# Kernel tuning notes

Hardware: AMD Instinct MI355X
Metric: run time of the kernel (lower is better)

The kernel has to match this reference:

```python
import jax, jax.numpy as jnp
import numpy as np

N_HEAD = 16
ROPE_BASE = 10000.0


def _rope_tables(T, head_dim, dtype):
    # RotaryEmbedding(dim=head_dim//2): inv_freq over arange(0, dim, 2)/dim
    rot = head_dim // 2  # 32
    inv_freq = 1.0 / (ROPE_BASE ** (jnp.arange(0, rot, 2, dtype=jnp.float32) / rot))  # [rot/2]
    pos = jnp.arange(T, dtype=jnp.float32)
    freqs = jnp.outer(pos, inv_freq)                     # [T, rot/2]
    emb = jnp.concatenate([freqs, freqs], axis=-1)       # [T, rot]
    return jnp.cos(emb).astype(dtype), jnp.sin(emb).astype(dtype)


def _apply_rope(q, k, cos, sin):
    # q,k: [B,H,T,hd]; cos,sin: [T, hd//2] broadcast over B,H
    hd = q.shape[-1]
    half = hd // 2
    cos = cos[None, None]
    sin = sin[None, None]
    q1, q2 = q[..., :half], q[..., half:]
    k1, k2 = k[..., :half], k[..., half:]
    q_rot = jnp.concatenate([q1 * cos - q2 * sin, q2 * cos + q1 * sin], axis=-1)
    k_rot = jnp.concatenate([k1 * cos - k2 * sin, k2 * cos + k1 * sin], axis=-1)
    return q_rot, k_rot


def setup_inputs() -> dict:
    key = jax.random.key(0)
    ks = jax.random.split(key, 4)
    B, T, C = 4, 2048, 1024
    x = jax.random.normal(ks[0], (B, T, C), dtype=jnp.float32)
    W_attn = jax.random.normal(ks[1], (C, 3 * C), dtype=jnp.float32) * (1.0 / np.sqrt(C))
    b_attn = jnp.zeros((3 * C,), dtype=jnp.float32)
    W_proj = jax.random.normal(ks[2], (C, C), dtype=jnp.float32) * (1.0 / np.sqrt(C))
    b_proj = jnp.zeros((C,), dtype=jnp.float32)
    return {"x": x, "W_attn": W_attn, "b_attn": b_attn, "W_proj": W_proj, "b_proj": b_proj}


def reference(x, W_attn, b_attn, W_proj, b_proj):
    B, T, C = x.shape
    H = N_HEAD
    hd = C // H
    qkv = x @ W_attn + b_attn                            # [B,T,3C]
    q, k, v = jnp.split(qkv, 3, axis=-1)
    # [B,T,C] -> [B,H,T,hd]
    q = q.reshape(B, T, H, hd).transpose(0, 2, 1, 3)
    k = k.reshape(B, T, H, hd).transpose(0, 2, 1, 3)
    v = v.reshape(B, T, H, hd).transpose(0, 2, 1, 3)
    cos, sin = _rope_tables(T, hd, x.dtype)
    q, k = _apply_rope(q, k, cos, sin)
    att = jnp.einsum("bhqd,bhkd->bhqk", q, k) * (1.0 / np.sqrt(hd))
    causal = jnp.tril(jnp.ones((T, T), dtype=bool))
    att = jnp.where(causal[None, None], att, jnp.float32(-jnp.inf).astype(att.dtype))
    att = jax.nn.softmax(att, axis=-1)
    y = jnp.einsum("bhqk,bhkd->bhqd", att, v)            # [B,H,T,hd]
    y = y.transpose(0, 2, 1, 3).reshape(B, T, C)
    return y @ W_proj + b_proj
```

## Files before the change

kernel.cpp:

```cpp
#include <hip/hip_runtime.h>
#include <math.h>


typedef unsigned short u16;
typedef __bf16 bf16x8 __attribute__((ext_vector_type(8)));
typedef float f32x4 __attribute__((ext_vector_type(4)));
typedef float f32x16 __attribute__((ext_vector_type(16)));

__device__ __forceinline__ float b2f(u16 x) {
  union { unsigned u; float f; } c; c.u = ((unsigned)x) << 16; return c.f;
}
__device__ __forceinline__ u16 f2b(float f) {
  union { __bf16 h; u16 u; } c; c.h = (__bf16)f; return c.u;
}

__global__ __launch_bounds__(256) void sentinel_k(u16* __restrict__ out, int n) {
  int i = blockIdx.x * 256 + threadIdx.x;
  if (i < n) out[i] = 0x4480;
}

__global__ __launch_bounds__(256) void transpose_f2b_k(const float* __restrict__ src,
                                                       u16* __restrict__ dst,
                                                       int R, int C) {
  __shared__ u16 tile[64][65];
  int tc = blockIdx.x * 64, tr = blockIdx.y * 64;
  int t = threadIdx.x;
  int rr = t >> 3;
  int c8 = (t & 7) * 8;
#pragma unroll
  for (int i = 0; i < 2; ++i) {
    int r = rr + i * 32;
    f32x4 p0 = *(const f32x4*)(src + (long)(tr + r) * C + tc + c8);
    f32x4 p1 = *(const f32x4*)(src + (long)(tr + r) * C + tc + c8 + 4);
#pragma unroll
    for (int j = 0; j < 4; ++j) {
      tile[r][c8 + j] = f2b(p0[j]);
      tile[r][c8 + 4 + j] = f2b(p1[j]);
    }
  }
  __syncthreads();
#pragma unroll
  for (int i = 0; i < 2; ++i) {
    int a = rr + i * 32;
    u16 vv[8];
#pragma unroll
    for (int j = 0; j < 8; ++j) vv[j] = tile[c8 + j][a];
    *(uint4*)(dst + (long)(tc + a) * R + tr + c8) = *(uint4*)vv;
  }
}

__global__ __launch_bounds__(256) void transpose_b_k(const u16* __restrict__ src,
                                                     u16* __restrict__ dst,
                                                     int R, int C,
                                                     long sBatch, long dBatch) {
  __shared__ u16 tile[64][65];
  src += (long)blockIdx.z * sBatch;
  dst += (long)blockIdx.z * dBatch;
  int tc = blockIdx.x * 64, tr = blockIdx.y * 64;
  int t = threadIdx.x;
  int rr = t >> 3;
  int c8 = (t & 7) * 8;
#pragma unroll
  for (int i = 0; i < 2; ++i) {
    int r = rr + i * 32;
    uint4 v = *(const uint4*)(src + (long)(tr + r) * C + tc + c8);
    u16 vv[8]; *(uint4*)vv = v;
#pragma unroll
    for (int j = 0; j < 8; ++j) tile[r][c8 + j] = vv[j];
  }
  __syncthreads();
#pragma unroll
  for (int i = 0; i < 2; ++i) {
    int a = rr + i * 32;
    u16 vv[8];
#pragma unroll
    for (int j = 0; j < 8; ++j) vv[j] = tile[c8 + j][a];
    *(uint4*)(dst + (long)(tc + a) * R + tr + c8) = *(uint4*)vv;
  }
}

__global__ void rope_table_k(float2* __restrict__ tab) {
  int i = blockIdx.x * 256 + threadIdx.x;
  if (i >= 2048 * 16) return;
  int t = i >> 4, f = i & 15;
  float invf = exp2f(-(float)f * (13.287712379549449f / 16.0f));
  float th = (float)t * invf;
  float s, c;
  sincosf(th, &s, &c);
  tab[i] = make_float2(c, s);
}

__global__ __launch_bounds__(256) void rope_apply_k(u16* __restrict__ Qg,
                                                    u16* __restrict__ Kg,
                                                    const float2* __restrict__ tab) {
  const float QSCALE = 0.18033688501389543f;
  long tid = (long)blockIdx.x * 256 + threadIdx.x;
  int j = (int)(tid & 7);
  long row = tid >> 3;
  int t = (int)(row & 2047);
  int d0 = j * 4;
  u16* qp = Qg + row * 64;
  u16* kp = Kg + row * 64;
  u16 a1[4], a2[4], b1[4], b2[4];
  *(ushort4*)a1 = *(ushort4*)(qp + d0);
  *(ushort4*)a2 = *(ushort4*)(qp + d0 + 32);
  *(ushort4*)b1 = *(ushort4*)(kp + d0);
  *(ushort4*)b2 = *(ushort4*)(kp + d0 + 32);
  const float2* tp = tab + t * 16 + (d0 & 15);
#pragma unroll
  for (int i = 0; i < 4; ++i) {
    float2 cs = tp[i];
    float x1 = b2f(a1[i]), x2 = b2f(a2[i]);
    float y1 = b2f(b1[i]), y2 = b2f(b2[i]);
    a1[i] = f2b((x1 * cs.x - x2 * cs.y) * QSCALE);
    a2[i] = f2b((x2 * cs.x + x1 * cs.y) * QSCALE);
    b1[i] = f2b(y1 * cs.x - y2 * cs.y);
    b2[i] = f2b(y2 * cs.x + y1 * cs.y);
  }
  *(ushort4*)(qp + d0) = *(ushort4*)a1;
  *(ushort4*)(qp + d0 + 32) = *(ushort4*)a2;
  *(ushort4*)(kp + d0) = *(ushort4*)b1;
  *(ushort4*)(kp + d0 + 32) = *(ushort4*)b2;
}

template <int MODE>
__global__ __launch_bounds__(256) void gemm_k(const void* __restrict__ Av,
                                              const u16* __restrict__ Bt,
                                              const float* __restrict__ bias,
                                              void* __restrict__ outv,
                                              int M, int N, int K) {
  __shared__ u16 As[128 * 40];
  __shared__ u16 Bs[128 * 40];
  int tid = threadIdx.x, wid = tid >> 6, lane = tid & 63;
  int wr = wid >> 1, wc = wid & 1;
  long m0 = (long)blockIdx.x * 128, n0 = (long)blockIdx.y * 128;
  int r = lane & 15, g = lane >> 4;
  long arow = m0 + wid * 32 + (lane >> 2);
  int acol = (lane & 3) * 8;
  const float* Agf = (const float*)Av + arow * (long)K + acol;
  const u16*   Agb = (const u16*)Av + arow * (long)K + acol;
  const u16* Bg = Bt + (n0 + wid * 32 + (lane >> 2)) * (long)K + acol;
  int lrow = wid * 32 + (lane >> 2);
  int lcol = acol;
  f32x4 acc[4][4] = {};
  int nk = K >> 5;
  for (int kt = 0; kt < nk; ++kt) {
    long ko = (long)kt * 32;
    uint4 a0, a1;
    if (MODE == 1) {
      f32x4 p0 = *(const f32x4*)(Agf + ko);
      f32x4 p1 = *(const f32x4*)(Agf + ko + 4);
      f32x4 p2 = *(const f32x4*)(Agf + ko + 16 * (long)K);
      f32x4 p3 = *(const f32x4*)(Agf + ko + 16 * (long)K + 4);
      u16 h0[8], h1[8];
#pragma unroll
      for (int j = 0; j < 4; ++j) {
        h0[j] = f2b(p0[j]); h0[4 + j] = f2b(p1[j]);
        h1[j] = f2b(p2[j]); h1[4 + j] = f2b(p3[j]);
      }
      a0 = *(uint4*)h0; a1 = *(uint4*)h1;
    } else {
      a0 = *(const uint4*)(Agb + ko);
      a1 = *(const uint4*)(Agb + ko + 16 * (long)K);
    }
    uint4 b0 = *(const uint4*)(Bg + ko);
    uint4 b1 = *(const uint4*)(Bg + ko + 16 * (long)K);
    __syncthreads();
    *(uint4*)&As[lrow * 40 + lcol] = a0;
    *(uint4*)&As[(lrow + 16) * 40 + lcol] = a1;
    *(uint4*)&Bs[lrow * 40 + lcol] = b0;
    *(uint4*)&Bs[(lrow + 16) * 40 + lcol] = b1;
    __syncthreads();
    bf16x8 af[4], bfr[4];
#pragma unroll
    for (int mt = 0; mt < 4; ++mt)
      af[mt] = *(const bf16x8*)&As[(wr * 64 + mt * 16 + r) * 40 + g * 8];
#pragma unroll
    for (int nt = 0; nt < 4; ++nt)
      bfr[nt] = *(const bf16x8*)&Bs[(wc * 64 + nt * 16 + r) * 40 + g * 8];
#pragma unroll
    for (int mt = 0; mt < 4; ++mt)
#pragma unroll
      for (int nt = 0; nt < 4; ++nt)
        acc[mt][nt] = __builtin_amdgcn_mfma_f32_16x16x32_bf16(af[mt], bfr[nt], acc[mt][nt], 0, 0, 0);
  }
#pragma unroll
  for (int nt = 0; nt < 4; ++nt) {
    long col = n0 + wc * 64 + nt * 16 + r;
    float bv = bias[col];
#pragma unroll
    for (int mt = 0; mt < 4; ++mt) {
#pragma unroll
      for (int e = 0; e < 4; ++e) {
        long row = m0 + wr * 64 + mt * 16 + g * 4 + e;
        float v = acc[mt][nt][e] + bv;
        if (MODE == 0) {
          ((float*)outv)[row * N + col] = v;
        } else {
          int which = (int)(col >> 10);
          int cc = (int)col & 1023;
          int hh = cc >> 6, dd = cc & 63;
          long bb = row >> 11;
          int tt = (int)row & 2047;
          ((u16*)outv)[(long)which * 8388608 + (((bb * 16 + hh) * 2048 + tt) << 6) + dd] = f2b(v);
        }
      }
    }
  }
}

__global__ __launch_bounds__(256) void attn_k(const u16* __restrict__ Qg,
                                              const u16* __restrict__ Kg,
                                              const u16* __restrict__ VgT,
                                              u16* __restrict__ Y) {
  __shared__ u16 Ks[64 * 72];
  __shared__ u16 Vt[64 * 72];
  int qb = 15 - (int)blockIdx.y;
  int bh = blockIdx.x;
  int b = bh >> 4, h = bh & 15;
  long base = (long)bh * (2048 * 64);
  int tid = threadIdx.x, wid = tid >> 6;
  int lane = tid & 63, l31 = lane & 31, hi = lane >> 5;
  int q0w = qb * 128 + wid * 32;
  int myEnd = (q0w + 31) >> 6;
  int ktMax = 2 * qb + 1;
  bf16x8 qf[4];
  {
    const u16* qp = Qg + base + (long)(q0w + l31) * 64 + hi * 8;
#pragma unroll
    for (int s = 0; s < 4; ++s) qf[s] = *(const bf16x8*)(qp + s * 16);
  }
  f32x16 acc0 = {}, acc1 = {};
  float mrow = -INFINITY, lrow = 0.f;
  for (int kt = 0; kt <= ktMax; ++kt) {
    __syncthreads();
#pragma unroll
    for (int uu = 0; uu < 2; ++uu) {
      int u = tid + uu * 256;
      int row = u >> 3, c4 = (u & 7) * 8;
      *(uint4*)&Ks[row * 72 + c4] =
          *(const uint4*)&Kg[base + (long)(kt * 64 + row) * 64 + c4];
      *(uint4*)&Vt[row * 72 + c4] =
          *(const uint4*)&VgT[base + (long)row * 2048 + kt * 64 + c4];
    }
    __syncthreads();
    if (kt > myEnd) continue;
    f32x16 st[2];
#pragma unroll
    for (int ct = 0; ct < 2; ++ct) {
      f32x16 z = {};
#pragma unroll
      for (int s = 0; s < 4; ++s) {
        bf16x8 kf = *(const bf16x8*)&Ks[(ct * 32 + l31) * 72 + s * 16 + hi * 8];
        z = __builtin_amdgcn_mfma_f32_32x32x16_bf16(kf, qf[s], z, 0, 0, 0);
      }
      st[ct] = z;
    }
    if (kt == myEnd) {
      int qg = q0w + l31;
#pragma unroll
      for (int ct = 0; ct < 2; ++ct)
#pragma unroll
        for (int reg = 0; reg < 16; ++reg) {
          int kg = kt * 64 + ct * 32 + (reg & 3) + 8 * (reg >> 2) + 4 * hi;
          if (kg > qg) st[ct][reg] = -INFINITY;
        }
    }
    float t8[8];
#pragma unroll
    for (int i = 0; i < 8; ++i)
      t8[i] = fmaxf(fmaxf(st[0][i], st[0][i + 8]), fmaxf(st[1][i], st[1][i + 8]));
#pragma unroll
    for (int i = 0; i < 4; ++i) t8[i] = fmaxf(t8[i], t8[i + 4]);
    float pm = fmaxf(fmaxf(t8[0], t8[1]), fmaxf(t8[2], t8[3]));
    pm = fmaxf(pm, __shfl_xor(pm, 32));
    if (__any(pm > mrow + 8.0f)) {
      float mn = fmaxf(mrow, pm);
      float alpha = exp2f(mrow - mn);
      mrow = mn;
      lrow *= alpha;
#pragma unroll
      for (int reg = 0; reg < 16; ++reg) {
        float aB = __shfl(alpha, (reg & 3) + 8 * (reg >> 2) + 4 * hi);
        acc0[reg] *= aB;
        acc1[reg] *= aB;
      }
    }
    float s8[8];
#pragma unroll
    for (int i = 0; i < 8; ++i) s8[i] = 0.f;
#pragma unroll
    for (int ct = 0; ct < 2; ++ct)
#pragma unroll
      for (int reg = 0; reg < 16; ++reg) {
        float p = exp2f(st[ct][reg] - mrow);
        st[ct][reg] = p;
        s8[reg & 7] += p;
      }
#pragma unroll
    for (int i = 0; i < 4; ++i) s8[i] += s8[i + 4];
    float rs = (s8[0] + s8[1]) + (s8[2] + s8[3]);
    rs += __shfl_xor(rs, 32);
    lrow += rs;
#pragma unroll
    for (int ct = 0; ct < 2; ++ct) {
      bf16x8 af[2];
#pragma unroll
      for (int ks = 0; ks < 2; ++ks) {
#pragma unroll
        for (int u = 0; u < 4; ++u) {
          float sendv = hi ? st[ct][8 * ks + u] : st[ct][8 * ks + 4 + u];
          float keepv = hi ? st[ct][8 * ks + 4 + u] : st[ct][8 * ks + u];
          float rcv = __shfl_xor(sendv, 32);
          af[ks][u] = (__bf16)(hi ? rcv : keepv);
          af[ks][4 + u] = (__bf16)(hi ? keepv : rcv);
        }
      }
#pragma unroll
      for (int ks = 0; ks < 2; ++ks) {
        bf16x8 vf0 = *(const bf16x8*)&Vt[l31 * 72 + ct * 32 + ks * 16 + hi * 8];
        bf16x8 vf1 = *(const bf16x8*)&Vt[(32 + l31) * 72 + ct * 32 + ks * 16 + hi * 8];
        acc0 = __builtin_amdgcn_mfma_f32_32x32x16_bf16(af[ks], vf0, acc0, 0, 0, 0);
        acc1 = __builtin_amdgcn_mfma_f32_32x32x16_bf16(af[ks], vf1, acc1, 0, 0, 0);
      }
    }
  }
  float rinv = 1.0f / lrow;
#pragma unroll
  for (int reg = 0; reg < 16; ++reg) {
    int crow = (reg & 3) + 8 * (reg >> 2) + 4 * hi;
    float rB = __shfl(rinv, crow);
    long orow = (long)(b * 2048 + q0w + crow) * 1024 + h * 64;
    Y[orow + l31] = f2b(acc0[reg] * rB);
    Y[orow + 32 + l31] = f2b(acc1[reg] * rB);
  }
}

extern "C" void kernel_launch(void* const* d_in, const int* in_sizes, int n_in,
                              void* d_out, int out_size, void* d_ws, size_t ws_size,
                              hipStream_t stream) {
  const float* x  = (const float*)d_in[0];
  const float* Wa = (const float*)d_in[1];
  const float* ba = (const float*)d_in[2];
  const float* Wp = (const float*)d_in[3];
  const float* bp = (const float*)d_in[4];

  if (ws_size < 67108864ULL) {
    sentinel_k<<<dim3((out_size + 255) / 256), 256, 0, stream>>>((u16*)d_out, out_size);
    return;
  }

  u16* ws  = (u16*)d_ws;
  u16* Qg  = ws;
  u16* Kg  = ws + 8388608;
  u16* Vg  = ws + 16777216;
  u16* Yb  = ws + 16777216;
  u16* WaT = ws + 25165824;
  float2* tab = (float2*)(ws + 28311552);
  u16* VgT = ws + 25165824;
  u16* WpT = ws;

  transpose_f2b_k<<<dim3(48, 16), 256, 0, stream>>>(Wa, WaT, 1024, 3072);
  rope_table_k<<<dim3(128), 256, 0, stream>>>(tab);
  gemm_k<1><<<dim3(64, 24), 256, 0, stream>>>(x, WaT, ba, Qg, 8192, 3072, 1024);
  rope_apply_k<<<dim3(4096), 256, 0, stream>>>(Qg, Kg, tab);
  transpose_b_k<<<dim3(1, 32, 64), 256, 0, stream>>>(Vg, VgT, 2048, 64, 131072L, 131072L);
  attn_k<<<dim3(64, 16), 256, 0, stream>>>(Qg, Kg, VgT, Yb);
  transpose_f2b_k<<<dim3(16, 16), 256, 0, stream>>>(Wp, WpT, 1024, 1024);
  gemm_k<0><<<dim3(64, 8), 256, 0, stream>>>(Yb, WpT, bp, d_out, 8192, 1024, 1024);
}
```

Before: 224.9 us.

## Fuse RoPE into QKV GEMM, pair causal q-strips, use direct-to-LDS loads

Folds the RoPE rotation and Q scaling into the QKV GEMM epilogue, which removes the separate rope_apply pass that read and rewrote Q and K. The attention kernel now gives each wave two 32-row query strips, one near the start and one near the end of the sequence, to balance causal work across blocks, and halves the grid. The output projection GEMM switches to global_load_lds for direct global-to-LDS copies with an unpadded layout. The risks are LDS bank conflicts from dropping the padding, higher register pressure in attention, and an extra barrier per k-step in the projection GEMM.

```diff
diff --git a/kernel.cpp b/kernel.cpp
--- a/kernel.cpp
+++ b/kernel.cpp
@@ -7,12 +7,19 @@
 typedef float f32x4 __attribute__((ext_vector_type(4)));
 typedef float f32x16 __attribute__((ext_vector_type(16)));
 
+#define QSCALE 0.18033688501389543f
+
 __device__ __forceinline__ float b2f(u16 x) {
   union { unsigned u; float f; } c; c.u = ((unsigned)x) << 16; return c.f;
 }
 __device__ __forceinline__ u16 f2b(float f) {
   union { __bf16 h; u16 u; } c; c.h = (__bf16)f; return c.u;
 }
+
+#define GLOAD16(gp, lp)                                                  \
+  __builtin_amdgcn_global_load_lds(                                      \
+      (const __attribute__((address_space(1))) unsigned int*)(gp),       \
+      (__attribute__((address_space(3))) unsigned int*)(lp), 16, 0, 0)
 
 __global__ __launch_bounds__(256) void sentinel_k(u16* __restrict__ out, int n) {
   int i = blockIdx.x * 256 + threadIdx.x;
@@ -90,45 +97,12 @@
   tab[i] = make_float2(c, s);
 }
 
-__global__ __launch_bounds__(256) void rope_apply_k(u16* __restrict__ Qg,
-                                                    u16* __restrict__ Kg,
-                                                    const float2* __restrict__ tab) {
-  const float QSCALE = 0.18033688501389543f;
-  long tid = (long)blockIdx.x * 256 + threadIdx.x;
-  int j = (int)(tid & 7);
-  long row = tid >> 3;
-  int t = (int)(row & 2047);
-  int d0 = j * 4;
-  u16* qp = Qg + row * 64;
-  u16* kp = Kg + row * 64;
-  u16 a1[4], a2[4], b1[4], b2[4];
-  *(ushort4*)a1 = *(ushort4*)(qp + d0);
-  *(ushort4*)a2 = *(ushort4*)(qp + d0 + 32);
-  *(ushort4*)b1 = *(ushort4*)(kp + d0);
-  *(ushort4*)b2 = *(ushort4*)(kp + d0 + 32);
-  const float2* tp = tab + t * 16 + (d0 & 15);
-#pragma unroll
-  for (int i = 0; i < 4; ++i) {
-    float2 cs = tp[i];
-    float x1 = b2f(a1[i]), x2 = b2f(a2[i]);
-    float y1 = b2f(b1[i]), y2 = b2f(b2[i]);
-    a1[i] = f2b((x1 * cs.x - x2 * cs.y) * QSCALE);
-    a2[i] = f2b((x2 * cs.x + x1 * cs.y) * QSCALE);
-    b1[i] = f2b(y1 * cs.x - y2 * cs.y);
-    b2[i] = f2b(y2 * cs.x + y1 * cs.y);
-  }
-  *(ushort4*)(qp + d0) = *(ushort4*)a1;
-  *(ushort4*)(qp + d0 + 32) = *(ushort4*)a2;
-  *(ushort4*)(kp + d0) = *(ushort4*)b1;
-  *(ushort4*)(kp + d0 + 32) = *(ushort4*)b2;
-}
-
-template <int MODE>
-__global__ __launch_bounds__(256) void gemm_k(const void* __restrict__ Av,
-                                              const u16* __restrict__ Bt,
-                                              const float* __restrict__ bias,
-                                              void* __restrict__ outv,
-                                              int M, int N, int K) {
+__global__ __launch_bounds__(256) void gemm_qkv_k(const float* __restrict__ A,
+                                                  const u16* __restrict__ Bt,
+                                                  const float* __restrict__ bias,
+                                                  const float2* __restrict__ tab,
+                                                  u16* __restrict__ out,
+                                                  int M, int N, int K) {
   __shared__ u16 As[128 * 40];
   __shared__ u16 Bs[128 * 40];
   int tid = threadIdx.x, wid = tid >> 6, lane = tid & 63;
@@ -137,8 +111,7 @@
   int r = lane & 15, g = lane >> 4;
   long arow = m0 + wid * 32 + (lane >> 2);
   int acol = (lane & 3) * 8;
-  const float* Agf = (const float*)Av + arow * (long)K + acol;
-  const u16*   Agb = (const u16*)Av + arow * (long)K + acol;
+  const float* Agf = A + arow * (long)K + acol;
   const u16* Bg = Bt + (n0 + wid * 32 + (lane >> 2)) * (long)K + acol;
   int lrow = wid * 32 + (lane >> 2);
   int lcol = acol;
@@ -146,23 +119,17 @@
   int nk = K >> 5;
   for (int kt = 0; kt < nk; ++kt) {
     long ko = (long)kt * 32;
-    uint4 a0, a1;
-    if (MODE == 1) {
-      f32x4 p0 = *(const f32x4*)(Agf + ko);
-      f32x4 p1 = *(const f32x4*)(Agf + ko + 4);
-      f32x4 p2 = *(const f32x4*)(Agf + ko + 16 * (long)K);
-      f32x4 p3 = *(const f32x4*)(Agf + ko + 16 * (long)K + 4);
-      u16 h0[8], h1[8];
-#pragma unroll
-      for (int j = 0; j < 4; ++j) {
-        h0[j] = f2b(p0[j]); h0[4 + j] = f2b(p1[j]);
-        h1[j] = f2b(p2[j]); h1[4 + j] = f2b(p3[j]);
-      }
-      a0 = *(uint4*)h0; a1 = *(uint4*)h1;
-    } else {
-      a0 = *(const uint4*)(Agb + ko);
-      a1 = *(const uint4*)(Agb + ko + 16 * (long)K);
-    }
+    f32x4 p0 = *(const f32x4*)(Agf + ko);
+    f32x4 p1 = *(const f32x4*)(Agf + ko + 4);
+    f32x4 p2 = *(const f32x4*)(Agf + ko + 16 * (long)K);
+    f32x4 p3 = *(const f32x4*)(Agf + ko + 16 * (long)K + 4);
+    u16 h0[8], h1[8];
+#pragma unroll
+    for (int j = 0; j < 4; ++j) {
+      h0[j] = f2b(p0[j]); h0[4 + j] = f2b(p1[j]);
+      h1[j] = f2b(p2[j]); h1[4 + j] = f2b(p3[j]);
+    }
+    uint4 a0 = *(uint4*)h0, a1 = *(uint4*)h1;
     uint4 b0 = *(const uint4*)(Bg + ko);
     uint4 b1 = *(const uint4*)(Bg + ko + 16 * (long)K);
     __syncthreads();
@@ -184,55 +151,119 @@
       for (int nt = 0; nt < 4; ++nt)
         acc[mt][nt] = __builtin_amdgcn_mfma_f32_16x16x32_bf16(af[mt], bfr[nt], acc[mt][nt], 0, 0, 0);
   }
+  int which = (int)(n0 >> 10);
+  int hh = ((int)(n0 & 1023) >> 6) + wc;
+  float bv[4];
+#pragma unroll
+  for (int nt = 0; nt < 4; ++nt) bv[nt] = bias[n0 + wc * 64 + nt * 16 + r];
+#pragma unroll
+  for (int mt = 0; mt < 4; ++mt) {
+#pragma unroll
+    for (int e = 0; e < 4; ++e) {
+      long row = m0 + wr * 64 + mt * 16 + g * 4 + e;
+      long bb = row >> 11;
+      int tt = (int)row & 2047;
+      float v0 = acc[mt][0][e] + bv[0];
+      float v1 = acc[mt][1][e] + bv[1];
+      float v2 = acc[mt][2][e] + bv[2];
+      float v3 = acc[mt][3][e] + bv[3];
+      if (which < 2) {
+        float2 cs = tab[tt * 16 + r];
+        float r0 = v0 * cs.x - v2 * cs.y, r2 = v2 * cs.x + v0 * cs.y;
+        float r1 = v1 * cs.x - v3 * cs.y, r3 = v3 * cs.x + v1 * cs.y;
+        if (which == 0) { r0 *= QSCALE; r1 *= QSCALE; r2 *= QSCALE; r3 *= QSCALE; }
+        v0 = r0; v1 = r1; v2 = r2; v3 = r3;
+      }
+      u16* op = out + (long)which * 8388608 + (((bb * 16 + hh) * 2048 + tt) << 6);
+      op[r] = f2b(v0);
+      op[16 + r] = f2b(v1);
+      op[32 + r] = f2b(v2);
+      op[48 + r] = f2b(v3);
+    }
+  }
+}
+
+__global__ __launch_bounds__(256) void gemm_proj_k(const u16* __restrict__ A,
+                                                   const u16* __restrict__ Bt,
+                                                   const float* __restrict__ bias,
+                                                   float* __restrict__ out,
+                                                   int M, int N, int K) {
+  __shared__ u16 As[128 * 32];
+  __shared__ u16 Bs[128 * 32];
+  int tid = threadIdx.x, wid = tid >> 6, lane = tid & 63;
+  int wr = wid >> 1, wc = wid & 1;
+  long m0 = (long)blockIdx.x * 128, n0 = (long)blockIdx.y * 128;
+  int r = lane & 15, g = lane >> 4;
+  const u16* Ag = A + (m0 + wid * 32 + (lane >> 2)) * (long)K + (lane & 3) * 8;
+  const u16* Bg = Bt + (n0 + wid * 32 + (lane >> 2)) * (long)K + (lane & 3) * 8;
+  u16* AsW = As + wid * 1024;
+  u16* BsW = Bs + wid * 1024;
+  f32x4 acc[4][4] = {};
+  int nk = K >> 5;
+  for (int kt = 0; kt < nk; ++kt) {
+    long ko = (long)kt * 32;
+    GLOAD16(Ag + ko, AsW);
+    GLOAD16(Ag + ko + 16 * (long)K, AsW + 512);
+    GLOAD16(Bg + ko, BsW);
+    GLOAD16(Bg + ko + 16 * (long)K, BsW + 512);
+    __syncthreads();
+    bf16x8 af[4], bfr[4];
+#pragma unroll
+    for (int mt = 0; mt < 4; ++mt)
+      af[mt] = *(const bf16x8*)&As[(wr * 64 + mt * 16 + r) * 32 + g * 8];
+#pragma unroll
+    for (int nt = 0; nt < 4; ++nt)
+      bfr[nt] = *(const bf16x8*)&Bs[(wc * 64 + nt * 16 + r) * 32 + g * 8];
+#pragma unroll
+    for (int mt = 0; mt < 4; ++mt)
+#pragma unroll
+      for (int nt = 0; nt < 4; ++nt)
+        acc[mt][nt] = __builtin_amdgcn_mfma_f32_16x16x32_bf16(af[mt], bfr[nt], acc[mt][nt], 0, 0, 0);
+    __syncthreads();
+  }
 #pragma unroll
   for (int nt = 0; nt < 4; ++nt) {
     long col = n0 + wc * 64 + nt * 16 + r;
-    float bv = bias[col];
-#pragma unroll
-    for (int mt = 0; mt < 4; ++mt) {
+    float bvv = bias[col];
+#pragma unroll
+    for (int mt = 0; mt < 4; ++mt)
 #pragma unroll
       for (int e = 0; e < 4; ++e) {
         long row = m0 + wr * 64 + mt * 16 + g * 4 + e;
-        float v = acc[mt][nt][e] + bv;
-        if (MODE == 0) {
-          ((float*)outv)[row * N + col] = v;
-        } else {
-          int which = (int)(col >> 10);
-          int cc = (int)col & 1023;
-          int hh = cc >> 6, dd = cc & 63;
-          long bb = row >> 11;
-          int tt = (int)row & 2047;
-          ((u16*)outv)[(long)which * 8388608 + (((bb * 16 + hh) * 2048 + tt) << 6) + dd] = f2b(v);
-        }
-      }
-    }
-  }
-}
-
-__global__ __launch_bounds__(256) void attn_k(const u16* __restrict__ Qg,
-                                              const u16* __restrict__ Kg,
-                                              const u16* __restrict__ VgT,
-                                              u16* __restrict__ Y) {
+        out[row * N + col] = acc[mt][nt][e] + bvv;
+      }
+  }
+}
+
+__global__ __launch_bounds__(256, 2) void attn_k(const u16* __restrict__ Qg,
+                                                 const u16* __restrict__ Kg,
+                                                 const u16* __restrict__ VgT,
+                                                 u16* __restrict__ Y) {
   __shared__ u16 Ks[64 * 72];
   __shared__ u16 Vt[64 * 72];
-  int qb = 15 - (int)blockIdx.y;
+  int ib = blockIdx.y;
   int bh = blockIdx.x;
   int b = bh >> 4, h = bh & 15;
   long base = (long)bh * (2048 * 64);
   int tid = threadIdx.x, wid = tid >> 6;
   int lane = tid & 63, l31 = lane & 31, hi = lane >> 5;
-  int q0w = qb * 128 + wid * 32;
-  int myEnd = (q0w + 31) >> 6;
-  int ktMax = 2 * qb + 1;
-  bf16x8 qf[4];
+  int sA = ib * 4 + wid, sB = 63 - sA;
+  int q0A = sA * 32, q0B = sB * 32;
+  int endA = sA >> 1, endB = sB >> 1;
+  int ktEnd = 31 - 2 * ib;
+  bf16x8 qfA[4], qfB[4];
   {
-    const u16* qp = Qg + base + (long)(q0w + l31) * 64 + hi * 8;
-#pragma unroll
-    for (int s = 0; s < 4; ++s) qf[s] = *(const bf16x8*)(qp + s * 16);
-  }
-  f32x16 acc0 = {}, acc1 = {};
-  float mrow = -INFINITY, lrow = 0.f;
-  for (int kt = 0; kt <= ktMax; ++kt) {
+    const u16* qa = Qg + base + (long)(q0A + l31) * 64 + hi * 8;
+    const u16* qb = Qg + base + (long)(q0B + l31) * 64 + hi * 8;
+#pragma unroll
+    for (int s = 0; s < 4; ++s) {
+      qfA[s] = *(const bf16x8*)(qa + s * 16);
+      qfB[s] = *(const bf16x8*)(qb + s * 16);
+    }
+  }
+  f32x16 accA0 = {}, accA1 = {}, accB0 = {}, accB1 = {};
+  float mA = -INFINITY, lA = 0.f, mB = -INFINITY, lB = 0.f;
+  for (int kt = 0; kt <= ktEnd; ++kt) {
     __syncthreads();
 #pragma unroll
     for (int uu = 0; uu < 2; ++uu) {
@@ -244,96 +275,104 @@
           *(const uint4*)&VgT[base + (long)row * 2048 + kt * 64 + c4];
     }
     __syncthreads();
-    if (kt > myEnd) continue;
-    f32x16 st[2];
-#pragma unroll
-    for (int ct = 0; ct < 2; ++ct) {
-      f32x16 z = {};
-#pragma unroll
-      for (int s = 0; s < 4; ++s) {
-        bf16x8 kf = *(const bf16x8*)&Ks[(ct * 32 + l31) * 72 + s * 16 + hi * 8];
-        z = __builtin_amdgcn_mfma_f32_32x32x16_bf16(kf, qf[s], z, 0, 0, 0);
-      }
-      st[ct] = z;
-    }
-    if (kt == myEnd) {
-      int qg = q0w + l31;
+    auto tileC = [&](const bf16x8 (&qf)[4], f32x16& acc0, f32x16& acc1,
+                     float& mrow, float& lrow, int q0, int endS) {
+      f32x16 st[2];
+#pragma unroll
+      for (int ct = 0; ct < 2; ++ct) {
+        f32x16 z = {};
+#pragma unroll
+        for (int s = 0; s < 4; ++s) {
+          bf16x8 kf = *(const bf16x8*)&Ks[(ct * 32 + l31) * 72 + s * 16 + hi * 8];
+          z = __builtin_amdgcn_mfma_f32_32x32x16_bf16(kf, qf[s], z, 0, 0, 0);
+        }
+        st[ct] = z;
+      }
+      if (kt == endS) {
+        int qg = q0 + l31;
+#pragma unroll
+        for (int ct = 0; ct < 2; ++ct)
+#pragma unroll
+          for (int reg = 0; reg < 16; ++reg) {
+            int kg = kt * 64 + ct * 32 + (reg & 3) + 8 * (reg >> 2) + 4 * hi;
+            if (kg > qg) st[ct][reg] = -INFINITY;
+          }
+      }
+      float t8[8];
+#pragma unroll
+      for (int i = 0; i < 8; ++i)
+        t8[i] = fmaxf(fmaxf(st[0][i], st[0][i + 8]), fmaxf(st[1][i], st[1][i + 8]));
+#pragma unroll
+      for (int i = 0; i < 4; ++i) t8[i] = fmaxf(t8[i], t8[i + 4]);
+      float pm = fmaxf(fmaxf(t8[0], t8[1]), fmaxf(t8[2], t8[3]));
+      pm = fmaxf(pm, __shfl_xor(pm, 32));
+      if (__any(pm > mrow + 8.0f)) {
+        float mn = fmaxf(mrow, pm);
+        float alpha = exp2f(mrow - mn);
+        mrow = mn;
+        lrow *= alpha;
+#pragma unroll
+        for (int reg = 0; reg < 16; ++reg) {
+          float aB = __shfl(alpha, (reg & 3) + 8 * (reg >> 2) + 4 * hi);
+          acc0[reg] *= aB;
+          acc1[reg] *= aB;
+        }
+      }
+      float s8[8];
+#pragma unroll
+      for (int i = 0; i < 8; ++i) s8[i] = 0.f;
 #pragma unroll
       for (int ct = 0; ct < 2; ++ct)
 #pragma unroll
         for (int reg = 0; reg < 16; ++reg) {
-          int kg = kt * 64 + ct * 32 + (reg & 3) + 8 * (reg >> 2) + 4 * hi;
-          if (kg > qg) st[ct][reg] = -INFINITY;
+          float p = exp2f(st[ct][reg] - mrow);
+          st[ct][reg] = p;
+          s8[reg & 7] += p;
         }
-    }
-    float t8[8];
-#pragma unroll
-    for (int i = 0; i < 8; ++i)
-      t8[i] = fmaxf(fmaxf(st[0][i], st[0][i + 8]), fmaxf(st[1][i], st[1][i + 8]));
-#pragma unroll
-    for (int i = 0; i < 4; ++i) t8[i] = fmaxf(t8[i], t8[i + 4]);
-    float pm = fmaxf(fmaxf(t8[0], t8[1]), fmaxf(t8[2], t8[3]));
-    pm = fmaxf(pm, __shfl_xor(pm, 32));
-    if (__any(pm > mrow + 8.0f)) {
-      float mn = fmaxf(mrow, pm);
-      float alpha = exp2f(mrow - mn);
-      mrow = mn;
-      lrow *= alpha;
-#pragma unroll
-      for (int reg = 0; reg < 16; ++reg) {
-        float aB = __shfl(alpha, (reg & 3) + 8 * (reg >> 2) + 4 * hi);
-        acc0[reg] *= aB;
-        acc1[reg] *= aB;
-      }
-    }
-    float s8[8];
-#pragma unroll
-    for (int i = 0; i < 8; ++i) s8[i] = 0.f;
-#pragma unroll
-    for (int ct = 0; ct < 2; ++ct)
-#pragma unroll
-      for (int reg = 0; reg < 16; ++reg) {
-        float p = exp2f(st[ct][reg] - mrow);
-        st[ct][reg] = p;
-        s8[reg & 7] += p;
-      }
-#pragma unroll
-    for (int i = 0; i < 4; ++i) s8[i] += s8[i + 4];
-    float rs = (s8[0] + s8[1]) + (s8[2] + s8[3]);
-    rs += __shfl_xor(rs, 32);
-    lrow += rs;
-#pragma unroll
-    for (int ct = 0; ct < 2; ++ct) {
-      bf16x8 af[2];
-#pragma unroll
-      for (int ks = 0; ks < 2; ++ks) {
-#pragma unroll
-        for (int u = 0; u < 4; ++u) {
-          float sendv = hi ? st[ct][8 * ks + u] : st[ct][8 * ks + 4 + u];
-          float keepv = hi ? st[ct][8 * ks + 4 + u] : st[ct][8 * ks + u];
-          float rcv = __shfl_xor(sendv, 32);
-          af[ks][u] = (__bf16)(hi ? rcv : keepv);
-          af[ks][4 + u] = (__bf16)(hi ? keepv : rcv);
+#pragma unroll
+      for (int i = 0; i < 4; ++i) s8[i] += s8[i + 4];
+      float rs = (s8[0] + s8[1]) + (s8[2] + s8[3]);
+      rs += __shfl_xor(rs, 32);
+      lrow += rs;
+#pragma unroll
+      for (int ct = 0; ct < 2; ++ct) {
+        bf16x8 af[2];
+#pragma unroll
+        for (int ks = 0; ks < 2; ++ks) {
+#pragma unroll
+          for (int u = 0; u < 4; ++u) {
+            float sendv = hi ? st[ct][8 * ks + u] : st[ct][8 * ks + 4 + u];
+            float keepv = hi ? st[ct][8 * ks + 4 + u] : st[ct][8 * ks + u];
+            float rcv = __shfl_xor(sendv, 32);
+            af[ks][u] = (__bf16)(hi ? rcv : keepv);
+            af[ks][4 + u] = (__bf16)(hi ? keepv : rcv);
+          }
         }
-      }
-#pragma unroll
-      for (int ks = 0; ks < 2; ++ks) {
-        bf16x8 vf0 = *(const bf16x8*)&Vt[l31 * 72 + ct * 32 + ks * 16 + hi * 8];
-        bf16x8 vf1 = *(const bf16x8*)&Vt[(32 + l31) * 72 + ct * 32 + ks * 16 + hi * 8];
-        acc0 = __builtin_amdgcn_mfma_f32_32x32x16_bf16(af[ks], vf0, acc0, 0, 0, 0);
-        acc1 = __builtin_amdgcn_mfma_f32_32x32x16_bf16(af[ks], vf1, acc1, 0, 0, 0);
-      }
-    }
-  }
-  float rinv = 1.0f / lrow;
-#pragma unroll
-  for (int reg = 0; reg < 16; ++reg) {
-    int crow = (reg & 3) + 8 * (reg >> 2) + 4 * hi;
-    float rB = __shfl(rinv, crow);
-    long orow = (long)(b * 2048 + q0w + crow) * 1024 + h * 64;
-    Y[orow + l31] = f2b(acc0[reg] * rB);
-    Y[orow + 32 + l31] = f2b(acc1[reg] * rB);
-  }
+#pragma unroll
+        for (int ks = 0; ks < 2; ++ks) {
+          bf16x8 vf0 = *(const bf16x8*)&Vt[l31 * 72 + ct * 32 + ks * 16 + hi * 8];
+          bf16x8 vf1 = *(const bf16x8*)&Vt[(32 + l31) * 72 + ct * 32 + ks * 16 + hi * 8];
+          acc0 = __builtin_amdgcn_mfma_f32_32x32x16_bf16(af[ks], vf0, acc0, 0, 0, 0);
+          acc1 = __builtin_amdgcn_mfma_f32_32x32x16_bf16(af[ks], vf1, acc1, 0, 0, 0);
+        }
+      }
+    };
+    if (kt <= endA) tileC(qfA, accA0, accA1, mA, lA, q0A, endA);
+    if (kt <= endB) tileC(qfB, accB0, accB1, mB, lB, q0B, endB);
+  }
+  auto writeO = [&](const f32x16& acc0, const f32x16& acc1, float lrow, int q0) {
+    float rinv = 1.0f / lrow;
+#pragma unroll
+    for (int reg = 0; reg < 16; ++reg) {
+      int crow = (reg & 3) + 8 * (reg >> 2) + 4 * hi;
+      float rB = __shfl(rinv, crow);
+      long orow = (long)(b * 2048 + q0 + crow) * 1024 + h * 64;
+      Y[orow + l31] = f2b(acc0[reg] * rB);
+      Y[orow + 32 + l31] = f2b(acc1[reg] * rB);
+    }
+  };
+  writeO(accA0, accA1, lA, q0A);
+  writeO(accB0, accB1, lB, q0B);
 }
 
 extern "C" void kernel_launch(void* const* d_in, const int* in_sizes, int n_in,
@@ -362,10 +401,9 @@
 
   transpose_f2b_k<<<dim3(48, 16), 256, 0, stream>>>(Wa, WaT, 1024, 3072);
   rope_table_k<<<dim3(128), 256, 0, stream>>>(tab);
-  gemm_k<1><<<dim3(64, 24), 256, 0, stream>>>(x, WaT, ba, Qg, 8192, 3072, 1024);
-  rope_apply_k<<<dim3(4096), 256, 0, stream>>>(Qg, Kg, tab);
+  gemm_qkv_k<<<dim3(64, 24), 256, 0, stream>>>(x, WaT, ba, tab, Qg, 8192, 3072, 1024);
   transpose_b_k<<<dim3(1, 32, 64), 256, 0, stream>>>(Vg, VgT, 2048, 64, 131072L, 131072L);
-  attn_k<<<dim3(64, 16), 256, 0, stream>>>(Qg, Kg, VgT, Yb);
+  attn_k<<<dim3(64, 8), 256, 0, stream>>>(Qg, Kg, VgT, Yb);
   transpose_f2b_k<<<dim3(16, 16), 256, 0, stream>>>(Wp, WpT, 1024, 1024);
-  gemm_k<0><<<dim3(64, 8), 256, 0, stream>>>(Yb, WpT, bp, d_out, 8192, 1024, 1024);
-}
+  gemm_proj_k<<<dim3(64, 8), 256, 0, stream>>>(Yb, WpT, bp, (float*)d_out, 8192, 1024, 1024);
+}
```

Measured after the change: 211.2 us. 1.06x faster.
